# Performance work log

Hardware: AMD Instinct MI355X
Metric: run time of the kernel (lower is better)

Reference implementation:

```python
import jax, jax.numpy as jnp
import numpy as np

B, C, H, W = 8, 512, 32, 32
NH = 8


def setup_inputs() -> dict:
    key = jax.random.key(0)
    ks = jax.random.split(key, 10)
    s = 1.0 / np.sqrt(C)
    return {
        "query": jax.random.normal(ks[0], (B, C, H, W), jnp.float32),
        "key": jax.random.normal(ks[1], (B, C, H, W), jnp.float32),
        "Wq": jax.random.normal(ks[2], (C, C), jnp.float32) * s,
        "bq": jnp.zeros((C,), jnp.float32),
        "Wk": jax.random.normal(ks[3], (C, C), jnp.float32) * s,
        "bk": jnp.zeros((C,), jnp.float32),
        "Wv": jax.random.normal(ks[4], (C, C), jnp.float32) * s,
        "bv": jnp.zeros((C,), jnp.float32),
        "Wo": jax.random.normal(ks[5], (C, C), jnp.float32) * s,
        "bo": jnp.zeros((C,), jnp.float32),
        "num_heads": NH,
    }


def reference(query, key, Wq, bq, Wk, bk, Wv, bv, Wo, bo, num_heads):
    b, c, h, w = query.shape
    hd = c // num_heads
    scale = hd ** (-0.5)
    # [B,C,H,W] -> [B, L, C] with L = H*W
    qf = jnp.transpose(query, (0, 2, 3, 1)).reshape(b, -1, c)
    kf = jnp.transpose(key, (0, 2, 3, 1)).reshape(b, -1, c)
    L = qf.shape[1]
    # Linear projections (torch Linear: x @ W.T + b); value = key
    q = qf @ Wq.T + bq
    k = kf @ Wk.T + bk
    v = kf @ Wv.T + bv
    # split heads: [B, L, NH, hd] -> [B, NH, L, hd]
    q = q.reshape(b, L, num_heads, hd).transpose(0, 2, 1, 3) * scale
    k = k.reshape(b, L, num_heads, hd).transpose(0, 2, 1, 3)
    v = v.reshape(b, L, num_heads, hd).transpose(0, 2, 1, 3)
    scores = jnp.einsum('bhqd,bhkd->bhqk', q, k)
    attn = jax.nn.softmax(scores, axis=-1)  # dropout p=0.0 -> identity
    o = jnp.einsum('bhqk,bhkd->bhqd', attn, v)
    o = o.transpose(0, 2, 1, 3).reshape(b, L, c)
    o = o @ Wo.T + bo
    o = o + qf + kf  # residual with flattened query and key
    return jnp.transpose(o.reshape(b, h, w, c), (0, 3, 1, 2))
```

## Files before the change

kernel.cpp:

```cpp
#include <hip/hip_runtime.h>
#include <stdint.h>

#define B_  8
#define C_  512
#define L_  1024
#define NH_ 8
#define HD_ 64

typedef __attribute__((ext_vector_type(8))) short short8;
typedef __attribute__((ext_vector_type(4))) short short4v;
typedef __attribute__((ext_vector_type(4))) float f32x4;
typedef __attribute__((ext_vector_type(2))) unsigned uint2v;

#define MFMA(a,b,c) __builtin_amdgcn_mfma_f32_16x16x32_bf16((a),(b),(c),0,0,0)
#define GLD16(g,l) __builtin_amdgcn_global_load_lds( \
    (const __attribute__((address_space(1))) void*)(g), \
    (__attribute__((address_space(3))) void*)(l), 16, 0, 0)

__device__ __forceinline__ unsigned short f2bf(float f) {
  union { float f; unsigned u; } x; x.f = f;
  unsigned r = x.u + 0x7FFFu + ((x.u >> 16) & 1u);
  return (unsigned short)(r >> 16);
}

__device__ __forceinline__ unsigned cvtpk_bf16(float lo, float hi) {
  unsigned r;
  asm("v_cvt_pk_bf16_f32 %0, %1, %2" : "=v"(r) : "v"(lo), "v"(hi));
  return r;
}

__global__ __launch_bounds__(256) void k_transpose(
    const float* __restrict__ q, const float* __restrict__ k,
    unsigned short* __restrict__ qf, unsigned short* __restrict__ kf) {
  __shared__ float t[32][33];
  const int z = blockIdx.z;
  const int b = z >> 1;
  const float* src = (z & 1) ? k : q;
  unsigned short* dst = (z & 1) ? kf : qf;
  const int tx = threadIdx.x & 31;
  const int ty = threadIdx.x >> 5;
  const int l0 = blockIdx.x * 32;
  const int c0 = blockIdx.y * 32;
#pragma unroll
  for (int i = 0; i < 4; ++i)
    t[ty + 8*i][tx] = src[((size_t)b * C_ + c0 + ty + 8*i) * L_ + l0 + tx];
  __syncthreads();
#pragma unroll
  for (int i = 0; i < 4; ++i)
    dst[((size_t)b * L_ + l0 + ty + 8*i) * C_ + c0 + tx] = f2bf(t[tx][ty + 8*i]);
}

__global__ __launch_bounds__(256) void k_convw(
    const float* __restrict__ w0, const float* __restrict__ w1,
    const float* __restrict__ w2, const float* __restrict__ w3,
    unsigned short* __restrict__ dst) {
  const int z = blockIdx.y;
  const float* s = (z == 0) ? w0 : (z == 1) ? w1 : (z == 2) ? w2 : w3;
  unsigned short* d = dst + (size_t)z * (C_ * C_);
  const int i = (blockIdx.x * 256 + threadIdx.x) * 4;
  float4 v = *(const float4*)&s[i];
  short4v p;
  p[0] = (short)f2bf(v.x); p[1] = (short)f2bf(v.y);
  p[2] = (short)f2bf(v.z); p[3] = (short)f2bf(v.w);
  *(short4v*)&d[i] = p;
}

template<int MREP>
__device__ __forceinline__ void gemm_core(
    const unsigned short* __restrict__ A, const unsigned short* __restrict__ W,
    const float* __restrict__ bias, void* __restrict__ outp,
    const float* __restrict__ resQ, const float* __restrict__ resK,
    int mode, float scale, unsigned short* lA, unsigned short* lB,
    int tm, int tn) {
  const int lane = threadIdx.x & 63;
  const int wid  = threadIdx.x >> 6;
  const int wm = wid >> 1, wn = wid & 1;
  const int r16 = lane & 15;
  const int g4  = lane >> 4;

  f32x4 acc[MREP][4];
#pragma unroll
  for (int i = 0; i < MREP; ++i)
#pragma unroll
    for (int j = 0; j < 4; ++j) acc[i][j] = (f32x4){0.f, 0.f, 0.f, 0.f};

  for (int kt = 0; kt < C_; kt += 64) {
#pragma unroll
    for (int i = 0; i < MREP; ++i) {
      int chunk = wid * MREP + i;
      int row = chunk * 8 + (lane >> 3);
      int col = (lane & 7) * 8;
      GLD16(A + (size_t)(tm + row) * C_ + kt + col, &lA[chunk * 512]);
    }
#pragma unroll
    for (int i = 0; i < 4; ++i) {
      int chunk = wid * 4 + i;
      int row = chunk * 8 + (lane >> 3);
      int col = (lane & 7) * 8;
      GLD16(W + (size_t)(tn + row) * C_ + kt + col, &lB[chunk * 512]);
    }
    __syncthreads();
#pragma unroll
    for (int ks = 0; ks < 2; ++ks) {
      const int co = ks * 32 + g4 * 8;
      short8 af[MREP], bw[4];
#pragma unroll
      for (int i = 0; i < MREP; ++i)
        af[i] = *(const short8*)&lA[(wm*(MREP*16) + i*16 + r16) * 64 + co];
#pragma unroll
      for (int j = 0; j < 4; ++j) bw[j] = *(const short8*)&lB[(wn*64 + j*16 + r16) * 64 + co];
#pragma unroll
      for (int i = 0; i < MREP; ++i)
#pragma unroll
        for (int j = 0; j < 4; ++j) acc[i][j] = MFMA(af[i], bw[j], acc[i][j]);
    }
    __syncthreads();
  }

  if (mode <= 1) {
    unsigned short* out = (unsigned short*)outp;
#pragma unroll
    for (int i = 0; i < MREP; ++i)
#pragma unroll
      for (int j = 0; j < 4; ++j) {
        int c = tn + wn*64 + j*16 + r16;
        float bia = bias[c];
        int h = c >> 6, d = c & 63;
#pragma unroll
        for (int r = 0; r < 4; ++r) {
          int gm = tm + wm*(MREP*16) + i*16 + g4*4 + r;
          int b = gm >> 10, l = gm & 1023;
          out[(((size_t)b * NH_ + h) * L_ + l) * HD_ + d] = f2bf((acc[i][j][r] + bia) * scale);
        }
      }
  } else if (mode == 2) {
    unsigned short* out = (unsigned short*)outp;
#pragma unroll
    for (int i = 0; i < MREP; ++i)
#pragma unroll
      for (int j = 0; j < 4; ++j) {
        int c = tn + wn*64 + j*16 + r16;
        float bia = bias[c];
        int h = c >> 6, d = c & 63;
        int gm0 = tm + wm*(MREP*16) + i*16 + g4*4;
        int b = gm0 >> 10, l0 = gm0 & 1023;
        short4v pk;
#pragma unroll
        for (int r = 0; r < 4; ++r) pk[r] = (short)f2bf(acc[i][j][r] + bia);
        *(short4v*)&out[(((size_t)b * NH_ + h) * HD_ + d) * L_ + l0] = pk;
      }
  } else {
    float* out = (float*)outp;
#pragma unroll
    for (int i = 0; i < MREP; ++i)
#pragma unroll
      for (int j = 0; j < 4; ++j) {
        int c = tn + wn*64 + j*16 + r16;
        float bia = bias[c];
        int gm0 = tm + wm*(MREP*16) + i*16 + g4*4;
        int b = gm0 >> 10, l0 = gm0 & 1023;
        size_t idx = ((size_t)b * C_ + c) * L_ + l0;
        float4 q4 = *(const float4*)&resQ[idx];
        float4 k4 = *(const float4*)&resK[idx];
        float4 o4;
        o4.x = acc[i][j][0] + bia + q4.x + k4.x;
        o4.y = acc[i][j][1] + bia + q4.y + k4.y;
        o4.z = acc[i][j][2] + bia + q4.z + k4.z;
        o4.w = acc[i][j][3] + bia + q4.w + k4.w;
        *(float4*)&out[idx] = o4;
      }
  }
}

__global__ __launch_bounds__(256) void k_proj(
    const unsigned short* __restrict__ qf, const unsigned short* __restrict__ kf,
    const unsigned short* __restrict__ Wqb, const unsigned short* __restrict__ Wkb,
    const unsigned short* __restrict__ Wvb,
    const float* __restrict__ bq, const float* __restrict__ bk, const float* __restrict__ bv,
    unsigned short* __restrict__ Qw, unsigned short* __restrict__ Kw,
    unsigned short* __restrict__ VTw) {
  __shared__ unsigned short lA[128 * 64];
  __shared__ unsigned short lB[128 * 64];
  const int bid = blockIdx.x;
  const int xcd = bid & 7;
  const int i_  = bid >> 3;
  const int ml  = i_ / 12;
  const int rem = i_ - ml * 12;
  const int z   = rem >> 2;
  const int n   = rem & 3;
  const int m   = xcd * 8 + ml;
  const unsigned short* A = (z == 0) ? qf : kf;
  const unsigned short* W = (z == 0) ? Wqb : (z == 1) ? Wkb : Wvb;
  const float* bias = (z == 0) ? bq : (z == 1) ? bk : bv;
  void* out = (z == 0) ? (void*)Qw : (z == 1) ? (void*)Kw : (void*)VTw;
  float scale = (z == 0) ? 0.125f * 1.44269504088896f : 1.0f;
  gemm_core<4>(A, W, bias, out, nullptr, nullptr, z, scale, lA, lB, m * 128, n * 128);
}

__global__ __launch_bounds__(256) void k_outproj(
    const unsigned short* __restrict__ O, const unsigned short* __restrict__ Wob,
    const float* __restrict__ bo, float* __restrict__ out,
    const float* __restrict__ query, const float* __restrict__ key) {
  __shared__ unsigned short lA[64 * 64];
  __shared__ unsigned short lB[128 * 64];
  const int bid = blockIdx.x;
  const int xcd = bid & 7;
  const int i_  = bid >> 3;
  const int m   = xcd * 16 + (i_ >> 2);
  const int n   = i_ & 3;
  gemm_core<2>(O, Wob, bo, out, query, key, 3, 1.0f, lA, lB, m * 64, n * 128);
}

__global__ __launch_bounds__(256, 4) void k_attn(
    const unsigned short* __restrict__ Q, const unsigned short* __restrict__ K,
    const unsigned short* __restrict__ VT, unsigned short* __restrict__ O) {
  __shared__ unsigned short Kt[2][64 * 64];
  __shared__ unsigned short Vt[2][64 * 64];
  __shared__ __align__(16) unsigned short Pl[4][16 * 36];
  const int lane = threadIdx.x & 63;
  const int wid  = threadIdx.x >> 6;
  const int bid  = blockIdx.x;
  const int xcd  = bid & 7;
  const int i_   = bid >> 3;
  const int bh   = xcd * 8 + (i_ >> 4);
  const int qb   = i_ & 15;
  const int qrow0 = qb * 64 + wid * 16;
  const int r16 = lane & 15;
  const int g4  = lane >> 4;
  const size_t base = (size_t)bh * L_ * HD_;
  const unsigned short* Kg = K + base;
  const unsigned short* Vg = VT + base;

  const int s0 = wid * 128 + lane;
  const int row0 = s0 >> 3,        ch0 = (s0 & 7) ^ (row0 & 7);
  const int row1 = (s0 + 64) >> 3, ch1 = ((s0 + 64) & 7) ^ (row1 & 7);

#define STAGE_KV(nxt, kt0) { \
    GLD16(Kg + (size_t)((kt0) + row0) * HD_ + ch0 * 8, &Kt[nxt][(wid*128)*8]); \
    GLD16(Kg + (size_t)((kt0) + row1) * HD_ + ch1 * 8, &Kt[nxt][(wid*128+64)*8]); \
    GLD16(Vg + (size_t)row0 * L_ + (kt0) + ch0 * 8, &Vt[nxt][(wid*128)*8]); \
    GLD16(Vg + (size_t)row1 * L_ + (kt0) + ch1 * 8, &Vt[nxt][(wid*128+64)*8]); \
  }

  short8 qv[2];
#pragma unroll
  for (int ks = 0; ks < 2; ++ks)
    qv[ks] = *(const short8*)(Q + base + (size_t)(qrow0 + r16) * HD_ + ks*32 + g4*8);

  short8 vones;
#pragma unroll
  for (int e = 0; e < 8; ++e) vones[e] = (short)0x3F80;

  f32x4 lacc = (f32x4){0.f, 0.f, 0.f, 0.f};
  f32x4 oacc[4];
#pragma unroll
  for (int j = 0; j < 4; ++j) oacc[j] = (f32x4){0.f, 0.f, 0.f, 0.f};

  unsigned short* myP = &Pl[wid][0];

  STAGE_KV(0, 0);
  __syncthreads();

  int cur = 0;
  for (int t = 0; t < 16; ++t) {
    if (t < 15) STAGE_KV(cur ^ 1, (t + 1) * 64);

    const unsigned short* lK = &Kt[cur][0];
    const unsigned short* lV = &Vt[cur][0];

    f32x4 sc[4];
#pragma unroll
    for (int cf = 0; cf < 4; ++cf) sc[cf] = (f32x4){0.f, 0.f, 0.f, 0.f};

    const int swz = r16 & 7;
    __builtin_amdgcn_s_setprio(1);
#pragma unroll
    for (int cf = 0; cf < 4; ++cf) {
      const int rowb = (cf*16 + r16) * 64;
      short8 kb0 = *(const short8*)&lK[rowb + ((g4) ^ swz) * 8];
      short8 kb1 = *(const short8*)&lK[rowb + ((4 + g4) ^ swz) * 8];
      sc[cf] = MFMA(kb0, qv[0], sc[cf]);
      sc[cf] = MFMA(kb1, qv[1], sc[cf]);
    }
    __builtin_amdgcn_s_setprio(0);

#pragma unroll
    for (int half = 0; half < 2; ++half) {
#pragma unroll
      for (int cfl = 0; cfl < 2; ++cfl) {
        const int cf = half * 2 + cfl;
        float p0 = exp2f(sc[cf][0]);
        float p1 = exp2f(sc[cf][1]);
        float p2 = exp2f(sc[cf][2]);
        float p3 = exp2f(sc[cf][3]);
        uint2v pk;
        pk[0] = cvtpk_bf16(p0, p1);
        pk[1] = cvtpk_bf16(p2, p3);
        *(uint2v*)&myP[r16 * 36 + cfl * 16 + g4 * 4] = pk;
      }
      short8 pa = *(const short8*)&myP[r16 * 36 + g4 * 8];
      __builtin_amdgcn_s_setprio(1);
      lacc = MFMA(pa, vones, lacc);
#pragma unroll
      for (int j = 0; j < 4; ++j) {
        short8 vb = *(const short8*)&lV[(j*16 + r16) * 64 + ((half*4 + g4) ^ swz) * 8];
        oacc[j] = MFMA(pa, vb, oacc[j]);
      }
      __builtin_amdgcn_s_setprio(0);
    }

    __syncthreads();
    cur ^= 1;
  }

  const int b = bh >> 3, h = bh & 7;
  float linv[4];
#pragma unroll
  for (int r = 0; r < 4; ++r) linv[r] = 1.0f / lacc[r];
#pragma unroll
  for (int j = 0; j < 4; ++j)
#pragma unroll
    for (int r = 0; r < 4; ++r) {
      int row = qrow0 + g4*4 + r;
      int col = h*64 + j*16 + r16;
      O[((size_t)b * L_ + row) * C_ + col] = f2bf(oacc[j][r] * linv[r]);
    }
#undef STAGE_KV
}

extern "C" void kernel_launch(void* const* d_in, const int* in_sizes, int n_in,
                              void* d_out, int out_size, void* d_ws, size_t ws_size,
                              hipStream_t stream) {
  (void)in_sizes; (void)n_in; (void)out_size; (void)ws_size;
  const float* query = (const float*)d_in[0];
  const float* key   = (const float*)d_in[1];
  const float* Wq = (const float*)d_in[2];
  const float* bq = (const float*)d_in[3];
  const float* Wk = (const float*)d_in[4];
  const float* bk = (const float*)d_in[5];
  const float* Wv = (const float*)d_in[6];
  const float* bv = (const float*)d_in[7];
  const float* Wo = (const float*)d_in[8];
  const float* bo = (const float*)d_in[9];

  char* ws = (char*)d_ws;
  unsigned short* qf  = (unsigned short*)(ws);
  unsigned short* kf  = (unsigned short*)(ws + 8388608);
  unsigned short* Wqb = (unsigned short*)(ws + 16777216);
  unsigned short* Wkb = Wqb + 262144;
  unsigned short* Wvb = Wkb + 262144;
  unsigned short* Wob = Wvb + 262144;
  unsigned short* Qw  = (unsigned short*)(ws + 18874368);
  unsigned short* Kw  = (unsigned short*)(ws + 27262976);
  unsigned short* VTw = (unsigned short*)(ws + 35651584);
  unsigned short* Ow  = (unsigned short*)(ws + 44040192);

  k_transpose<<<dim3(32, 16, 16), 256, 0, stream>>>(query, key, qf, kf);
  k_convw<<<dim3(256, 4), 256, 0, stream>>>(Wq, Wk, Wv, Wo, Wqb);
  k_proj<<<dim3(768), 256, 0, stream>>>(qf, kf, Wqb, Wkb, Wvb, bq, bk, bv, Qw, Kw, VTw);
  k_attn<<<dim3(1024), 256, 0, stream>>>(Qw, Kw, VTw, Ow);
  k_outproj<<<dim3(512), 256, 0, stream>>>(Ow, Wob, bo, (float*)d_out, query, key);
}
```

Measured before the change: 100.0 us.

## Process 32 query rows per wave in attention to reuse K/V tiles

Each wave in the attention kernel now handles two 16-row query sub-tiles, so a block covers 128 queries instead of 64. The grid is halved and the per-block K/V staging is amortised over twice as many rows. Each K and V fragment read from LDS now feeds two MFMAs. This costs more registers per thread (the launch bound drops from 4 to 2 blocks per CU), and the halved block count leaves less parallelism to hide latency.

```diff
diff --git a/kernel.cpp b/kernel.cpp
--- a/kernel.cpp
+++ b/kernel.cpp
@@ -211,20 +211,20 @@
   gemm_core<2>(O, Wob, bo, out, query, key, 3, 1.0f, lA, lB, m * 64, n * 128);
 }
 
-__global__ __launch_bounds__(256, 4) void k_attn(
+__global__ __launch_bounds__(256, 2) void k_attn(
     const unsigned short* __restrict__ Q, const unsigned short* __restrict__ K,
     const unsigned short* __restrict__ VT, unsigned short* __restrict__ O) {
   __shared__ unsigned short Kt[2][64 * 64];
   __shared__ unsigned short Vt[2][64 * 64];
-  __shared__ __align__(16) unsigned short Pl[4][16 * 36];
+  __shared__ __align__(16) unsigned short Pl[4][32 * 36];
   const int lane = threadIdx.x & 63;
   const int wid  = threadIdx.x >> 6;
   const int bid  = blockIdx.x;
   const int xcd  = bid & 7;
   const int i_   = bid >> 3;
-  const int bh   = xcd * 8 + (i_ >> 4);
-  const int qb   = i_ & 15;
-  const int qrow0 = qb * 64 + wid * 16;
+  const int bh   = xcd * 8 + (i_ >> 3);
+  const int qb   = i_ & 7;
+  const int qrow0 = qb * 128 + wid * 32;
   const int r16 = lane & 15;
   const int g4  = lane >> 4;
   const size_t base = (size_t)bh * L_ * HD_;
@@ -242,19 +242,25 @@
     GLD16(Vg + (size_t)row1 * L_ + (kt0) + ch1 * 8, &Vt[nxt][(wid*128+64)*8]); \
   }
 
-  short8 qv[2];
-#pragma unroll
-  for (int ks = 0; ks < 2; ++ks)
-    qv[ks] = *(const short8*)(Q + base + (size_t)(qrow0 + r16) * HD_ + ks*32 + g4*8);
+  short8 qv[2][2];
+#pragma unroll
+  for (int i = 0; i < 2; ++i)
+#pragma unroll
+    for (int ks = 0; ks < 2; ++ks)
+      qv[i][ks] = *(const short8*)(Q + base + (size_t)(qrow0 + i*16 + r16) * HD_ + ks*32 + g4*8);
 
   short8 vones;
 #pragma unroll
   for (int e = 0; e < 8; ++e) vones[e] = (short)0x3F80;
 
-  f32x4 lacc = (f32x4){0.f, 0.f, 0.f, 0.f};
-  f32x4 oacc[4];
-#pragma unroll
-  for (int j = 0; j < 4; ++j) oacc[j] = (f32x4){0.f, 0.f, 0.f, 0.f};
+  f32x4 lacc[2];
+  f32x4 oacc[2][4];
+#pragma unroll
+  for (int i = 0; i < 2; ++i) {
+    lacc[i] = (f32x4){0.f, 0.f, 0.f, 0.f};
+#pragma unroll
+    for (int j = 0; j < 4; ++j) oacc[i][j] = (f32x4){0.f, 0.f, 0.f, 0.f};
+  }
 
   unsigned short* myP = &Pl[wid][0];
 
@@ -268,9 +274,11 @@
     const unsigned short* lK = &Kt[cur][0];
     const unsigned short* lV = &Vt[cur][0];
 
-    f32x4 sc[4];
-#pragma unroll
-    for (int cf = 0; cf < 4; ++cf) sc[cf] = (f32x4){0.f, 0.f, 0.f, 0.f};
+    f32x4 sc[2][4];
+#pragma unroll
+    for (int i = 0; i < 2; ++i)
+#pragma unroll
+      for (int cf = 0; cf < 4; ++cf) sc[i][cf] = (f32x4){0.f, 0.f, 0.f, 0.f};
 
     const int swz = r16 & 7;
     __builtin_amdgcn_s_setprio(1);
@@ -279,32 +287,39 @@
       const int rowb = (cf*16 + r16) * 64;
       short8 kb0 = *(const short8*)&lK[rowb + ((g4) ^ swz) * 8];
       short8 kb1 = *(const short8*)&lK[rowb + ((4 + g4) ^ swz) * 8];
-      sc[cf] = MFMA(kb0, qv[0], sc[cf]);
-      sc[cf] = MFMA(kb1, qv[1], sc[cf]);
+      sc[0][cf] = MFMA(kb0, qv[0][0], sc[0][cf]);
+      sc[0][cf] = MFMA(kb1, qv[0][1], sc[0][cf]);
+      sc[1][cf] = MFMA(kb0, qv[1][0], sc[1][cf]);
+      sc[1][cf] = MFMA(kb1, qv[1][1], sc[1][cf]);
     }
     __builtin_amdgcn_s_setprio(0);
 
 #pragma unroll
     for (int half = 0; half < 2; ++half) {
 #pragma unroll
-      for (int cfl = 0; cfl < 2; ++cfl) {
-        const int cf = half * 2 + cfl;
-        float p0 = exp2f(sc[cf][0]);
-        float p1 = exp2f(sc[cf][1]);
-        float p2 = exp2f(sc[cf][2]);
-        float p3 = exp2f(sc[cf][3]);
-        uint2v pk;
-        pk[0] = cvtpk_bf16(p0, p1);
-        pk[1] = cvtpk_bf16(p2, p3);
-        *(uint2v*)&myP[r16 * 36 + cfl * 16 + g4 * 4] = pk;
-      }
-      short8 pa = *(const short8*)&myP[r16 * 36 + g4 * 8];
+      for (int i = 0; i < 2; ++i)
+#pragma unroll
+        for (int cfl = 0; cfl < 2; ++cfl) {
+          const int cf = half * 2 + cfl;
+          float p0 = exp2f(sc[i][cf][0]);
+          float p1 = exp2f(sc[i][cf][1]);
+          float p2 = exp2f(sc[i][cf][2]);
+          float p3 = exp2f(sc[i][cf][3]);
+          uint2v pk;
+          pk[0] = cvtpk_bf16(p0, p1);
+          pk[1] = cvtpk_bf16(p2, p3);
+          *(uint2v*)&myP[(i*16 + r16) * 36 + cfl * 16 + g4 * 4] = pk;
+        }
+      short8 pa0 = *(const short8*)&myP[r16 * 36 + g4 * 8];
+      short8 pa1 = *(const short8*)&myP[(16 + r16) * 36 + g4 * 8];
       __builtin_amdgcn_s_setprio(1);
-      lacc = MFMA(pa, vones, lacc);
+      lacc[0] = MFMA(pa0, vones, lacc[0]);
+      lacc[1] = MFMA(pa1, vones, lacc[1]);
 #pragma unroll
       for (int j = 0; j < 4; ++j) {
         short8 vb = *(const short8*)&lV[(j*16 + r16) * 64 + ((half*4 + g4) ^ swz) * 8];
-        oacc[j] = MFMA(pa, vb, oacc[j]);
+        oacc[0][j] = MFMA(pa0, vb, oacc[0][j]);
+        oacc[1][j] = MFMA(pa1, vb, oacc[1][j]);
       }
       __builtin_amdgcn_s_setprio(0);
     }
@@ -314,17 +329,20 @@
   }
 
   const int b = bh >> 3, h = bh & 7;
-  float linv[4];
-#pragma unroll
-  for (int r = 0; r < 4; ++r) linv[r] = 1.0f / lacc[r];
-#pragma unroll
-  for (int j = 0; j < 4; ++j)
-#pragma unroll
-    for (int r = 0; r < 4; ++r) {
-      int row = qrow0 + g4*4 + r;
-      int col = h*64 + j*16 + r16;
-      O[((size_t)b * L_ + row) * C_ + col] = f2bf(oacc[j][r] * linv[r]);
-    }
+#pragma unroll
+  for (int i = 0; i < 2; ++i) {
+    float linv[4];
+#pragma unroll
+    for (int r = 0; r < 4; ++r) linv[r] = 1.0f / lacc[i][r];
+#pragma unroll
+    for (int j = 0; j < 4; ++j)
+#pragma unroll
+      for (int r = 0; r < 4; ++r) {
+        int row = qrow0 + i*16 + g4*4 + r;
+        int col = h*64 + j*16 + r16;
+        O[((size_t)b * L_ + row) * C_ + col] = f2bf(oacc[i][j][r] * linv[r]);
+      }
+  }
 #undef STAGE_KV
 }
 
@@ -358,6 +376,6 @@
   k_transpose<<<dim3(32, 16, 16), 256, 0, stream>>>(query, key, qf, kf);
   k_convw<<<dim3(256, 4), 256, 0, stream>>>(Wq, Wk, Wv, Wo, Wqb);
   k_proj<<<dim3(768), 256, 0, stream>>>(qf, kf, Wqb, Wkb, Wvb, bq, bk, bv, Qw, Kw, VTw);
-  k_attn<<<dim3(1024), 256, 0, stream>>>(Qw, Kw, VTw, Ow);
+  k_attn<<<dim3(512), 256, 0, stream>>>(Qw, Kw, VTw, Ow);
   k_outproj<<<dim3(512), 256, 0, stream>>>(Ow, Wob, bo, (float*)d_out, query, key);
 }
```

Result: slower. 102.2 us (+2.2%).
